# Kernel tuning notes

Hardware: AMD Instinct MI355X
Metric: run time of the kernel (lower is better)

The kernel has to match this reference:

```python
import jax, jax.numpy as jnp
import numpy as np


def setup_inputs() -> dict:
    key = jax.random.key(0)
    ks = jax.random.split(key, 8)
    B, T, V, H = 32, 256, 1024, 1024
    scale_i = 1.0 / np.sqrt(V)   # lecun_normal-style init for dense kernels
    scale_h = 1.0 / np.sqrt(H)
    return {
        "c0": jax.random.normal(ks[0], (B, H), jnp.float32),
        "h0": jax.random.normal(ks[1], (B, H), jnp.float32),
        "inputs": jax.random.normal(ks[2], (B, T, V), jnp.float32),
        "Wi": jax.random.normal(ks[3], (V, 4 * H), jnp.float32) * scale_i,
        "Wh": jax.random.normal(ks[4], (H, 4 * H), jnp.float32) * scale_h,
        "b": jnp.zeros((4 * H,), jnp.float32),
        "Wd": jax.random.normal(ks[5], (H, V), jnp.float32) * scale_h,
        "bd": jnp.zeros((V,), jnp.float32),
    }


def reference(c0, h0, inputs, Wi, Wh, b, Wd, bd):
    # LSTM scanned over time axis (axis=1 of inputs), then Dense -> vocab.
    H = h0.shape[-1]

    def step(carry, x_t):  # x_t: [B, V]
        c, h = carry
        z = x_t @ Wi + h @ Wh + b            # [B, 4H], gates i,f,g,o
        i, f, g, o = jnp.split(z, 4, axis=-1)
        i = jax.nn.sigmoid(i)
        f = jax.nn.sigmoid(f)
        g = jnp.tanh(g)
        o = jax.nn.sigmoid(o)
        c = f * c + i * g
        h = o * jnp.tanh(c)
        return (c, h), h

    xs = jnp.swapaxes(inputs, 0, 1)          # [T, B, V]
    (c, h), hs = jax.lax.scan(step, (c0, h0), xs)
    outputs = jnp.swapaxes(hs, 0, 1)          # [B, T, H]
    x = outputs @ Wd + bd                     # [B, T, V]
    return (c, h, x)
```

## Files before the change

### kernel.cpp

```cpp
#include <hip/hip_runtime.h>
#include <cstdio>

typedef unsigned short u16;
typedef unsigned int u32;
typedef unsigned long long u64;
typedef __attribute__((ext_vector_type(8))) short bf16x8;
typedef __attribute__((ext_vector_type(4))) float f32x4;

#define NWG 128
#define FLAG_STRIDE 32

__device__ inline u16 f2bf(float x) {
  union { float f; unsigned u; } v; v.f = x;
  unsigned r = v.u + 0x7FFFu + ((v.u >> 16) & 1u);
  return (u16)(r >> 16);
}
__device__ inline float sigm(float x) { return 1.0f / (1.0f + __expf(-x)); }
__device__ inline float tanh_fast(float x) { return 1.0f - 2.0f / (__expf(2.0f * x) + 1.0f); }

__global__ __launch_bounds__(256) void k_convert(const float* __restrict__ in,
                                                 u16* __restrict__ out, int n4) {
  int i = blockIdx.x * blockDim.x + threadIdx.x;
  int stride = gridDim.x * blockDim.x;
  const float4* in4 = (const float4*)in;
  ushort4* out4 = (ushort4*)out;
  for (; i < n4; i += stride) {
    float4 v = in4[i];
    ushort4 o; o.x = f2bf(v.x); o.y = f2bf(v.y); o.z = f2bf(v.z); o.w = f2bf(v.w);
    out4[i] = o;
  }
}

__global__ __launch_bounds__(256) void k_init_h(const float* __restrict__ h0,
                                                u16* __restrict__ h_bf,
                                                u32* __restrict__ flags) {
  int i = blockIdx.x * blockDim.x + threadIdx.x;
  if (i < NWG * FLAG_STRIDE) flags[i] = 0u;
  if (i < 32768) h_bf[i] = f2bf(h0[i]);
}

__global__ __launch_bounds__(256) void k_transpose(const float* __restrict__ in,
                                                   u16* __restrict__ out, int R, int C) {
  __shared__ u16 tile[32][33];
  int tx = threadIdx.x & 31, ty = threadIdx.x >> 5;
  int c = blockIdx.x * 32 + tx;
  for (int i = 0; i < 32; i += 8) {
    int r = blockIdx.y * 32 + ty + i;
    tile[ty + i][tx] = f2bf(in[(size_t)r * C + c]);
  }
  __syncthreads();
  int r = blockIdx.y * 32 + tx;
  for (int i = 0; i < 32; i += 8) {
    int cc = blockIdx.x * 32 + ty + i;
    out[(size_t)cc * R + r] = tile[tx][ty + i];
  }
}

__global__ __launch_bounds__(256) void k_gemm_bt(const u16* __restrict__ A,
                                                 const u16* __restrict__ BT,
                                                 const float* __restrict__ bias,
                                                 float* __restrict__ C,
                                                 int M, int N, int K) {
  __shared__ u16 As[128][40];
  __shared__ u16 Bs[128][40];
  const int m0 = blockIdx.y * 128, n0 = blockIdx.x * 128;
  const int tid = threadIdx.x;
  const int lane = tid & 63, wave = tid >> 6;
  const int wm = (wave >> 1) * 64, wn = (wave & 1) * 64;
  const int lm = lane & 15, quad = lane >> 4;
  const int r = tid >> 1, kh = (tid & 1) * 16;

  f32x4 acc[4][4];
  for (int i = 0; i < 4; i++)
    for (int j = 0; j < 4; j++) acc[i][j] = (f32x4){0.f, 0.f, 0.f, 0.f};

  for (int k0 = 0; k0 < K; k0 += 32) {
    const uint4* ap = (const uint4*)(A + (size_t)(m0 + r) * K + k0 + kh);
    uint4 av0 = ap[0], av1 = ap[1];
    const uint4* bp = (const uint4*)(BT + (size_t)(n0 + r) * K + k0 + kh);
    uint4 bv0 = bp[0], bv1 = bp[1];
    __syncthreads();
    *(uint4*)&As[r][kh] = av0; *(uint4*)&As[r][kh + 8] = av1;
    *(uint4*)&Bs[r][kh] = bv0; *(uint4*)&Bs[r][kh + 8] = bv1;
    __syncthreads();
    bf16x8 a_frag[4], b_frag[4];
    for (int i = 0; i < 4; i++) a_frag[i] = *(const bf16x8*)&As[wm + i * 16 + lm][quad * 8];
    for (int j = 0; j < 4; j++) b_frag[j] = *(const bf16x8*)&Bs[wn + j * 16 + lm][quad * 8];
    for (int i = 0; i < 4; i++)
      for (int j = 0; j < 4; j++)
        acc[i][j] = __builtin_amdgcn_mfma_f32_16x16x32_bf16(a_frag[i], b_frag[j], acc[i][j], 0, 0, 0);
  }
  for (int i = 0; i < 4; i++)
    for (int j = 0; j < 4; j++) {
      int row = m0 + wm + i * 16 + quad * 4;
      int col = n0 + wn + j * 16 + lm;
      float bc = bias[col];
      for (int rr = 0; rr < 4; rr++)
        C[(size_t)(row + rr) * N + col] = acc[i][j][rr] + bc;
    }
}

__global__ __launch_bounds__(256) void k_lstm(const float* __restrict__ Z,
                                              const u16* __restrict__ WhT,
                                              const float* __restrict__ c0,
                                              u16* __restrict__ h_bf,
                                              u16* __restrict__ Hs,
                                              float* __restrict__ out_c,
                                              float* __restrict__ out_h,
                                              u32* __restrict__ flags) {
  __shared__ u16 Whs[32][1032];
  __shared__ u16 h_lds[32][1032];
  __shared__ float z_buf[32][34];
  const int g = blockIdx.x;
  const int tid = threadIdx.x;
  const int lane = tid & 63, wave = tid >> 6;
  const int lm = lane & 15, quad = lane >> 4;
  const int mhalf = wave >> 1, ntile = wave & 1;
  const int b = tid >> 3, jl = tid & 7;

  {
    int pc = tid >> 3, seg = tid & 7;
    int grow = (pc >> 3) * 1024 + 8 * g + (pc & 7);
    const uint4* src = (const uint4*)(WhT + (size_t)grow * 1024 + seg * 128);
#pragma unroll
    for (int i = 0; i < 16; i++) {
      uint4 v = src[i];
      *(uint4*)&Whs[pc][seg * 128 + i * 8] = v;
    }
  }
  float creg = c0[b * 1024 + 8 * g + jl];

  for (int t = 0; t < 256; t++) {
    size_t zbase = ((size_t)b * 256 + t) * 4096 + 8 * g + jl;
    float z_i = Z[zbase], z_f = Z[zbase + 1024], z_g = Z[zbase + 2048], z_o = Z[zbase + 3072];

    {
      const u32 tgt = (u32)t;
      const u32* f0 = flags + lane * FLAG_STRIDE;
      const u32* f1 = flags + (lane + 64) * FLAG_STRIDE;
      while (true) {
        u32 v0 = __hip_atomic_load(f0, __ATOMIC_RELAXED, __HIP_MEMORY_SCOPE_AGENT);
        u32 v1 = __hip_atomic_load(f1, __ATOMIC_RELAXED, __HIP_MEMORY_SCOPE_AGENT);
        if (__all((v0 >= tgt) && (v1 >= tgt))) break;
        __builtin_amdgcn_s_sleep(1);
      }
      asm volatile("" ::: "memory");
    }

    {
      const u64* hq = (const u64*)(h_bf + (size_t)(t & 1) * 32768);
      u64 v[32];
#pragma unroll
      for (int i = 0; i < 32; i++)
        v[i] = __hip_atomic_load(hq + i * 256 + tid, __ATOMIC_RELAXED, __HIP_MEMORY_SCOPE_AGENT);
#pragma unroll
      for (int i = 0; i < 32; i++) {
        int q = i * 256 + tid;
        *(u64*)&h_lds[q >> 8][(q & 255) * 4] = v[i];
      }
    }
    __syncthreads();

    const u16* arow = &h_lds[mhalf * 16 + lm][quad * 8];
    const u16* brow = &Whs[ntile * 16 + lm][quad * 8];
    f32x4 a0 = (f32x4){0.f, 0.f, 0.f, 0.f}, a1 = a0, a2 = a0, a3 = a0;
#pragma unroll
    for (int ks = 0; ks < 32; ks += 4) {
      bf16x8 af0 = *(const bf16x8*)(arow + (ks + 0) * 32);
      bf16x8 bf0 = *(const bf16x8*)(brow + (ks + 0) * 32);
      bf16x8 af1 = *(const bf16x8*)(arow + (ks + 1) * 32);
      bf16x8 bf1 = *(const bf16x8*)(brow + (ks + 1) * 32);
      bf16x8 af2 = *(const bf16x8*)(arow + (ks + 2) * 32);
      bf16x8 bf2 = *(const bf16x8*)(brow + (ks + 2) * 32);
      bf16x8 af3 = *(const bf16x8*)(arow + (ks + 3) * 32);
      bf16x8 bf3 = *(const bf16x8*)(brow + (ks + 3) * 32);
      a0 = __builtin_amdgcn_mfma_f32_16x16x32_bf16(af0, bf0, a0, 0, 0, 0);
      a1 = __builtin_amdgcn_mfma_f32_16x16x32_bf16(af1, bf1, a1, 0, 0, 0);
      a2 = __builtin_amdgcn_mfma_f32_16x16x32_bf16(af2, bf2, a2, 0, 0, 0);
      a3 = __builtin_amdgcn_mfma_f32_16x16x32_bf16(af3, bf3, a3, 0, 0, 0);
    }
    f32x4 accs = (a0 + a1) + (a2 + a3);
    for (int rr = 0; rr < 4; rr++)
      z_buf[mhalf * 16 + quad * 4 + rr][ntile * 16 + lm] = accs[rr];
    __syncthreads();

    float zi = z_buf[b][jl]      + z_i;
    float zf = z_buf[b][8 + jl]  + z_f;
    float zg = z_buf[b][16 + jl] + z_g;
    float zo = z_buf[b][24 + jl] + z_o;
    float ig = sigm(zi), fg = sigm(zf), gg = tanh_fast(zg), og = sigm(zo);
    creg = fg * creg + ig * gg;
    float hv = og * tanh_fast(creg);
    u16 hb = f2bf(hv);
    __hip_atomic_store(h_bf + (size_t)((t + 1) & 1) * 32768 + b * 1024 + 8 * g + jl,
                       hb, __ATOMIC_RELAXED, __HIP_MEMORY_SCOPE_AGENT);
    __builtin_nontemporal_store(hb, Hs + ((size_t)b * 256 + t) * 1024 + 8 * g + jl);
    if (t == 255) {
      out_c[b * 1024 + 8 * g + jl] = creg;
      out_h[b * 1024 + 8 * g + jl] = hv;
    }
    __syncthreads();
    if (tid == 0)
      __hip_atomic_store(flags + g * FLAG_STRIDE, (u32)(t + 1),
                         __ATOMIC_RELAXED, __HIP_MEMORY_SCOPE_AGENT);
  }
}

extern "C" void kernel_launch(void* const* d_in, const int* in_sizes, int n_in,
                              void* d_out, int out_size, void* d_ws, size_t ws_size,
                              hipStream_t stream) {
  const float* c0   = (const float*)d_in[0];
  const float* h0   = (const float*)d_in[1];
  const float* X    = (const float*)d_in[2];
  const float* Wi   = (const float*)d_in[3];
  const float* Wh   = (const float*)d_in[4];
  const float* bias = (const float*)d_in[5];
  const float* Wd   = (const float*)d_in[6];
  const float* bd   = (const float*)d_in[7];
  float* out   = (float*)d_out;
  float* out_c = out;
  float* out_h = out + 32768;
  float* out_x = out + 65536;

  char* ws = (char*)d_ws;
  size_t off = 0;
  auto alloc = [&](size_t bytes) { char* p = ws + off; off += (bytes + 255) & ~255ull; return p; };
  float* Z     = (float*)alloc(134217728ull);
  u16*   Xb    = (u16*)alloc(16777216ull);
  u16*   WiT   = (u16*)alloc(8388608ull);
  u16*   WhT   = (u16*)alloc(8388608ull);
  u16*   WdT   = (u16*)alloc(2097152ull);
  u16*   Hs    = (u16*)alloc(16777216ull);
  u16*   h_bf  = (u16*)alloc(131072ull);
  u32*   flags = (u32*)alloc(NWG * FLAG_STRIDE * 4);
  if (off > ws_size) {
    fprintf(stderr, "WS too small: need %zu have %zu\n", off, ws_size);
    return;
  }

  k_convert<<<2048, 256, 0, stream>>>(X, Xb, 8388608 / 4);
  k_init_h<<<128, 256, 0, stream>>>(h0, h_bf, flags);
  k_transpose<<<dim3(128, 32), 256, 0, stream>>>(Wi, WiT, 1024, 4096);
  k_transpose<<<dim3(128, 32), 256, 0, stream>>>(Wh, WhT, 1024, 4096);
  k_transpose<<<dim3(32, 32), 256, 0, stream>>>(Wd, WdT, 1024, 1024);
  k_gemm_bt<<<dim3(32, 64), 256, 0, stream>>>(Xb, WiT, bias, Z, 8192, 4096, 1024);
  k_lstm<<<NWG, 256, 0, stream>>>(Z, WhT, c0, h_bf, Hs, out_c, out_h, flags);
  k_gemm_bt<<<dim3(8, 64), 256, 0, stream>>>(Hs, WdT, bd, out_x, 8192, 1024, 1024);
}
```

Before: 1.187 ms.

## Replace per-block step barrier with per-wave tags and incremental h loading

Each wave now publishes its own progress tag after its h values are stored, removing the end-of-step __syncthreads and the single-thread flag store. Each thread polls only the four wave tags of the producer block whose h slice it reads, and loads those rows as soon as they are ready instead of waiting for all 128 blocks. The goal is to cut global barrier latency on the serial recurrence critical path and overlap h loads with straggler producers. It relies on relaxed atomics plus s_waitcnt for ordering, which carries memory-ordering risk, and uses more tag polling traffic.

```diff
diff --git a/kernel.cpp b/kernel.cpp
--- a/kernel.cpp
+++ b/kernel.cpp
@@ -8,7 +8,7 @@
 typedef __attribute__((ext_vector_type(4))) float f32x4;
 
 #define NWG 128
-#define FLAG_STRIDE 32
+#define TAG_STRIDE 8
 
 __device__ inline u16 f2bf(float x) {
   union { float f; unsigned u; } v; v.f = x;
@@ -33,9 +33,9 @@
 
 __global__ __launch_bounds__(256) void k_init_h(const float* __restrict__ h0,
                                                 u16* __restrict__ h_bf,
-                                                u32* __restrict__ flags) {
+                                                u32* __restrict__ tags) {
   int i = blockIdx.x * blockDim.x + threadIdx.x;
-  if (i < NWG * FLAG_STRIDE) flags[i] = 0u;
+  if (i < NWG * TAG_STRIDE) tags[i] = 0u;
   if (i < 32768) h_bf[i] = f2bf(h0[i]);
 }
 
@@ -107,7 +107,7 @@
                                               u16* __restrict__ Hs,
                                               float* __restrict__ out_c,
                                               float* __restrict__ out_h,
-                                              u32* __restrict__ flags) {
+                                              u32* __restrict__ tags) {
   __shared__ u16 Whs[32][1032];
   __shared__ u16 h_lds[32][1032];
   __shared__ float z_buf[32][34];
@@ -117,6 +117,7 @@
   const int lm = lane & 15, quad = lane >> 4;
   const int mhalf = wave >> 1, ntile = wave & 1;
   const int b = tid >> 3, jl = tid & 7;
+  const u32 myg = (u32)(tid >> 1);
 
   {
     int pc = tid >> 3, seg = tid & 7;
@@ -134,31 +135,39 @@
     size_t zbase = ((size_t)b * 256 + t) * 4096 + 8 * g + jl;
     float z_i = Z[zbase], z_f = Z[zbase + 1024], z_g = Z[zbase + 2048], z_o = Z[zbase + 3072];
 
-    {
-      const u32 tgt = (u32)t;
-      const u32* f0 = flags + lane * FLAG_STRIDE;
-      const u32* f1 = flags + (lane + 64) * FLAG_STRIDE;
-      while (true) {
-        u32 v0 = __hip_atomic_load(f0, __ATOMIC_RELAXED, __HIP_MEMORY_SCOPE_AGENT);
-        u32 v1 = __hip_atomic_load(f1, __ATOMIC_RELAXED, __HIP_MEMORY_SCOPE_AGENT);
-        if (__all((v0 >= tgt) && (v1 >= tgt))) break;
-        __builtin_amdgcn_s_sleep(1);
-      }
-      asm volatile("" ::: "memory");
-    }
-
+    u64 v[32];
     {
       const u64* hq = (const u64*)(h_bf + (size_t)(t & 1) * 32768);
-      u64 v[32];
-#pragma unroll
-      for (int i = 0; i < 32; i++)
-        v[i] = __hip_atomic_load(hq + i * 256 + tid, __ATOMIC_RELAXED, __HIP_MEMORY_SCOPE_AGENT);
-#pragma unroll
-      for (int i = 0; i < 32; i++) {
-        int q = i * 256 + tid;
-        *(u64*)&h_lds[q >> 8][(q & 255) * 4] = v[i];
+      const u32* tp = tags + myg * TAG_STRIDE;
+      const u32 tgt = (u32)t;
+      u32 pend = 0xFu;
+      while (pend) {
+        u32 got = 0;
+#pragma unroll
+        for (int w = 0; w < 4; w++)
+          if (pend & (1u << w)) {
+            u32 tv = __hip_atomic_load(tp + w, __ATOMIC_RELAXED, __HIP_MEMORY_SCOPE_AGENT);
+            if (tv >= tgt) got |= (1u << w);
+          }
+        if (got) {
+          asm volatile("" ::: "memory");
+#pragma unroll
+          for (int w = 0; w < 4; w++)
+            if (got & (1u << w)) {
+#pragma unroll
+              for (int j = 0; j < 8; j++)
+                v[w * 8 + j] = __hip_atomic_load(hq + (w * 8 + j) * 256 + tid,
+                                                 __ATOMIC_RELAXED, __HIP_MEMORY_SCOPE_AGENT);
+            }
+          pend &= ~got;
+        } else {
+          __builtin_amdgcn_s_sleep(1);
+        }
       }
     }
+#pragma unroll
+    for (int i = 0; i < 32; i++)
+      *(u64*)&h_lds[i][tid * 4] = v[i];
     __syncthreads();
 
     const u16* arow = &h_lds[mhalf * 16 + lm][quad * 8];
@@ -192,17 +201,19 @@
     creg = fg * creg + ig * gg;
     float hv = og * tanh_fast(creg);
     u16 hb = f2bf(hv);
+
     __hip_atomic_store(h_bf + (size_t)((t + 1) & 1) * 32768 + b * 1024 + 8 * g + jl,
                        hb, __ATOMIC_RELAXED, __HIP_MEMORY_SCOPE_AGENT);
+    asm volatile("s_waitcnt vmcnt(0)" ::: "memory");
+    if (lane == 0)
+      __hip_atomic_store(tags + g * TAG_STRIDE + wave, (u32)(t + 1),
+                         __ATOMIC_RELAXED, __HIP_MEMORY_SCOPE_AGENT);
+
     __builtin_nontemporal_store(hb, Hs + ((size_t)b * 256 + t) * 1024 + 8 * g + jl);
     if (t == 255) {
       out_c[b * 1024 + 8 * g + jl] = creg;
       out_h[b * 1024 + 8 * g + jl] = hv;
     }
-    __syncthreads();
-    if (tid == 0)
-      __hip_atomic_store(flags + g * FLAG_STRIDE, (u32)(t + 1),
-                         __ATOMIC_RELAXED, __HIP_MEMORY_SCOPE_AGENT);
   }
 }
 
@@ -232,18 +243,18 @@
   u16*   WdT   = (u16*)alloc(2097152ull);
   u16*   Hs    = (u16*)alloc(16777216ull);
   u16*   h_bf  = (u16*)alloc(131072ull);
-  u32*   flags = (u32*)alloc(NWG * FLAG_STRIDE * 4);
+  u32*   tags  = (u32*)alloc(NWG * TAG_STRIDE * 4);
   if (off > ws_size) {
     fprintf(stderr, "WS too small: need %zu have %zu\n", off, ws_size);
     return;
   }
 
   k_convert<<<2048, 256, 0, stream>>>(X, Xb, 8388608 / 4);
-  k_init_h<<<128, 256, 0, stream>>>(h0, h_bf, flags);
+  k_init_h<<<128, 256, 0, stream>>>(h0, h_bf, tags);
   k_transpose<<<dim3(128, 32), 256, 0, stream>>>(Wi, WiT, 1024, 4096);
   k_transpose<<<dim3(128, 32), 256, 0, stream>>>(Wh, WhT, 1024, 4096);
   k_transpose<<<dim3(32, 32), 256, 0, stream>>>(Wd, WdT, 1024, 1024);
   k_gemm_bt<<<dim3(32, 64), 256, 0, stream>>>(Xb, WiT, bias, Z, 8192, 4096, 1024);
-  k_lstm<<<NWG, 256, 0, stream>>>(Z, WhT, c0, h_bf, Hs, out_c, out_h, flags);
+  k_lstm<<<NWG, 256, 0, stream>>>(Z, WhT, c0, h_bf, Hs, out_c, out_h, tags);
   k_gemm_bt<<<dim3(8, 64), 256, 0, stream>>>(Hs, WdT, bd, out_x, 8192, 1024, 1024);
 }
```

Measured after the change: 1.419 ms. +19.6%, slower.
